# Kernel tuning notes

Measured on AMD Instinct MI355X. Metric: run time of the kernel, lower is better.

## Reference

```python
import jax, jax.numpy as jnp
import numpy as np

HEADS = 16
DIM_HEAD = 64
SCALE = 8.0
NUM_NULL_KV = 2
NON_CAUSAL_PREFIX = 64
LN_EPS = 1e-5

def _l2norm(t):
    # F.normalize: t / max(||t||_2, eps)
    n = jnp.sqrt(jnp.sum(t * t, axis=-1, keepdims=True))
    return t / jnp.maximum(n, 1e-12)

def _layer_norm(x, gamma):
    mu = jnp.mean(x, axis=-1, keepdims=True)
    var = jnp.mean((x - mu) ** 2, axis=-1, keepdims=True)
    return (x - mu) * jax.lax.rsqrt(var + LN_EPS) * gamma  # beta buffer is zeros

def setup_inputs() -> dict:
    key = jax.random.key(0)
    ks = jax.random.split(key, 6)
    b, n, dim = 2, 2048, 1024
    inner = HEADS * DIM_HEAD
    return {
        "x": jax.random.normal(ks[0], (b, n, dim), jnp.float32),
        "gamma": jnp.ones((dim,), jnp.float32),
        "Wq": jax.random.normal(ks[1], (dim, inner), jnp.float32) * (dim ** -0.5),
        "Wkv": jax.random.normal(ks[2], (dim, 2 * DIM_HEAD), jnp.float32) * (dim ** -0.5),
        "q_scale": jnp.ones((DIM_HEAD,), jnp.float32),
        "k_scale": jnp.ones((DIM_HEAD,), jnp.float32),
        "null_kv": jax.random.normal(ks[3], (2, NUM_NULL_KV, DIM_HEAD), jnp.float32),
        "Wout": jax.random.normal(ks[4], (inner, dim), jnp.float32) * (inner ** -0.5),
    }

def reference(x, gamma, Wq, Wkv, q_scale, k_scale, null_kv, Wout):
    b, n, dim = x.shape
    # NOTE: in the torch module, kv_input = x BEFORE self.norm is applied
    kv = jnp.einsum('bnd,de->bne', x, Wkv)          # [b, n, 2*dh]
    k, v = kv[..., :DIM_HEAD], kv[..., DIM_HEAD:]    # single shared kv head (MQA)
    xn = _layer_norm(x, gamma)
    q = jnp.einsum('bnd,de->bne', xn, Wq)            # [b, n, h*dh]
    # null kv prepended
    null_k = jnp.broadcast_to(null_kv[0], (b, NUM_NULL_KV, DIM_HEAD))
    null_v = jnp.broadcast_to(null_kv[1], (b, NUM_NULL_KV, DIM_HEAD))
    k = jnp.concatenate([null_k, k], axis=1)         # [b, j, dh]
    v = jnp.concatenate([null_v, v], axis=1)
    q = q.reshape(b, n, HEADS, DIM_HEAD).transpose(0, 2, 1, 3)  # [b, h, n, dh]
    q = _l2norm(q) * q_scale
    k = _l2norm(k) * k_scale
    sim = jnp.einsum('bhid,bjd->bhij', q, k) * SCALE  # [b, h, i, j]
    i, j = n, k.shape[1]
    rows = jnp.arange(i)[:, None]
    cols = jnp.arange(j)[None, :]
    causal_mask = cols > rows + (j - i)               # triu(j - i + 1)
    prefix_free = (rows < NON_CAUSAL_PREFIX) & (cols < NON_CAUSAL_PREFIX + (j - i))
    causal_mask = causal_mask & (~prefix_free)
    neg = -jnp.finfo(sim.dtype).max
    sim = jnp.where(causal_mask, neg, sim)
    attn = jax.nn.softmax(sim, axis=-1)
    out = jnp.einsum('bhij,bjd->bhid', attn, v)       # [b, h, n, dh]
    out = out.transpose(0, 2, 1, 3).reshape(b, n, HEADS * DIM_HEAD)
    return jnp.einsum('bne,ed->bnd', out, Wout)
```

## Files before the change

### kernel.cpp

```cpp
#include <hip/hip_runtime.h>

typedef _Float16 h16;
typedef _Float16 f16x8 __attribute__((ext_vector_type(8)));
typedef _Float16 f16x4 __attribute__((ext_vector_type(4)));
typedef float f32x4 __attribute__((ext_vector_type(4)));

#define KSCALE_FOLD 11.541560327111707f

#if __has_builtin(__builtin_amdgcn_exp2f)
#define EXP2(x) __builtin_amdgcn_exp2f(x)
#else
static __device__ __forceinline__ float EXP2(float x) {
    float r; asm("v_exp_f32 %0, %1" : "=v"(r) : "v"(x)); return r;
}
#endif

__global__ __launch_bounds__(256) void pre_k(const float* __restrict__ Wq,
    const float* __restrict__ Wkv, const float* __restrict__ Wout,
    const float* __restrict__ gamma, const float* __restrict__ x,
    const float* __restrict__ nkv, const float* __restrict__ kscale,
    h16* __restrict__ W1t, h16* __restrict__ Wot, float* __restrict__ cqp,
    float* __restrict__ mu, float* __restrict__ rr, h16* __restrict__ xh,
    h16* __restrict__ Kh, h16* __restrict__ Vth)
{
    __shared__ float ts[64][65];
    int pid = blockIdx.x;
    int tid = threadIdx.x;
    if (pid < 544) {
        int bx = pid & 15, by = pid >> 4;
        int c = tid & 63, rc = tid >> 6;
        const float* src; int ld, scol, drow0; h16* dst; bool useg = false;
        if (by < 16)      { src = Wq;   ld = 1024; scol = by*64;       dst = W1t; drow0 = scol;        useg = true; }
        else if (by < 18) { src = Wkv;  ld = 128;  scol = (by-16)*64;  dst = W1t; drow0 = 1024 + scol; }
        else              { src = Wout; ld = 1024; scol = (by-18)*64;  dst = Wot; drow0 = scol; }
        float part = 0.f;
#pragma unroll
        for (int i = 0; i < 16; ++i) {
            int r = rc*16 + i;
            float v = src[(size_t)(bx*64 + r)*ld + scol + c];
            if (useg) v *= gamma[bx*64 + r];
            part += v;
            ts[r][c] = v;
        }
        __syncthreads();
#pragma unroll
        for (int i = 0; i < 16; ++i) {
            int r = rc*16 + i;
            dst[(size_t)(drow0 + r)*1024 + bx*64 + c] = (h16)ts[c][r];
        }
        if (useg) {
            __syncthreads();
            ts[rc][c] = part;
            __syncthreads();
            if (rc == 0) {
                float s = ts[0][c] + ts[1][c] + ts[2][c] + ts[3][c];
                cqp[(size_t)bx*1024 + scol + c] = s;
            }
        }
    } else if (pid < 1568) {
        int w = tid >> 6, l = tid & 63;
        int row = (pid - 544)*4 + w;
        const float* xr = x + (size_t)row*1024;
        float s = 0.f, ss = 0.f;
        float4 v[4];
#pragma unroll
        for (int i = 0; i < 4; ++i) {
            v[i] = *(const float4*)(xr + i*256 + l*4);
            s  += v[i].x + v[i].y + v[i].z + v[i].w;
            ss += v[i].x*v[i].x + v[i].y*v[i].y + v[i].z*v[i].z + v[i].w*v[i].w;
        }
#pragma unroll
        for (int m = 1; m < 64; m <<= 1) { s += __shfl_xor(s, m); ss += __shfl_xor(ss, m); }
        float m_ = s * (1.f/1024.f);
        float var = ss * (1.f/1024.f) - m_*m_;
        float r_ = rsqrtf(var + 1e-5f);
        if (l == 0) { mu[row] = m_; rr[row] = r_; }
        h16* xo = xh + (size_t)row*1024;
#pragma unroll
        for (int i = 0; i < 4; ++i) {
            f16x4 hv = { (h16)v[i].x, (h16)v[i].y, (h16)v[i].z, (h16)v[i].w };
            *(f16x4*)(xo + i*256 + l*4) = hv;
        }
    } else {
        int nb = pid - 1568;
        if (nb == 0 && tid < 128) {
            int t = tid >> 6, d = tid & 63;
            float kv = nkv[(0*2 + t)*64 + d];
            float ss = kv*kv;
#pragma unroll
            for (int m = 1; m < 64; m <<= 1) ss += __shfl_xor(ss, m);
            float inv = 1.f / fmaxf(sqrtf(ss), 1e-12f);
            h16 kvh = (h16)(kv * inv * kscale[d] * KSCALE_FOLD);
            Kh[(size_t)(0*2112 + t)*64 + d] = kvh;
            Kh[(size_t)(1*2112 + t)*64 + d] = kvh;
            float nv = nkv[(2 + t)*64 + d];
            Vth[(size_t)(0*64 + d)*2112 + t] = (h16)nv;
            Vth[(size_t)(1*64 + d)*2112 + t] = (h16)nv;
        }
        for (int idx = nb*256 + tid; idx < 2*62*64; idx += 2048) {
            int b = idx / (62*64), rem = idx % (62*64);
            int j = 2050 + rem/64, d = rem & 63;
            Kh[((size_t)b*2112 + j)*64 + d] = (h16)0.f;
            Vth[((size_t)b*64 + d)*2112 + j] = (h16)0.f;
        }
    }
}

template<int MODE>
__global__ __launch_bounds__(256) void gemm_k(
    const h16* __restrict__ A, const h16* __restrict__ B,
    const float* __restrict__ mu, const float* __restrict__ rr, const float* __restrict__ cqp,
    const float* __restrict__ qscale, const float* __restrict__ kscale,
    h16* __restrict__ Qh, h16* __restrict__ Kh, h16* __restrict__ Vth, float* __restrict__ outp)
{
    __shared__ h16 As[2][128*64];
    __shared__ h16 Bs[2][64*64];
    int tid = threadIdx.x;
    int w = tid >> 6, l = tid & 63;
    int lq = l & 15, qq = l >> 4;
    int arow0 = blockIdx.y*128, bcol0 = blockIdx.x*64;
    const int K = 1024;
    f32x4 acc[2][4] = {};

    auto STAGE = [&](int buf, int kt) {
#pragma unroll
        for (int i = 0; i < 4; ++i) {
            int s = i*256 + tid;
            int row = s >> 3;
            int cb = ((s & 7)*16) ^ ((row & 7) << 4);
            const char* asrc = (const char*)(A + (size_t)(arow0 + row)*K + kt) + cb;
            __builtin_amdgcn_global_load_lds(
                (const __attribute__((address_space(1))) unsigned int*)asrc,
                (__attribute__((address_space(3))) unsigned int*)((char*)&As[buf][0] + s*16), 16, 0, 0);
        }
#pragma unroll
        for (int i = 0; i < 2; ++i) {
            int s = i*256 + tid;
            int row = s >> 3;
            int cb = ((s & 7)*16) ^ ((row & 7) << 4);
            const char* bsrc = (const char*)(B + (size_t)(bcol0 + row)*K + kt) + cb;
            __builtin_amdgcn_global_load_lds(
                (const __attribute__((address_space(1))) unsigned int*)bsrc,
                (__attribute__((address_space(3))) unsigned int*)((char*)&Bs[buf][0] + s*16), 16, 0, 0);
        }
    };

    STAGE(0, 0);
    int cur = 0;
    for (int kt = 0; kt < K; kt += 64) {
        int nkt = (kt + 64 < K) ? kt + 64 : kt;
        STAGE(cur ^ 1, nkt);
        asm volatile("s_waitcnt vmcnt(6)" ::: "memory");
        __builtin_amdgcn_s_barrier();
        __builtin_amdgcn_sched_barrier(0);
        const char* Ab = (const char*)&As[cur][0];
        const char* Bb = (const char*)&Bs[cur][0];
#pragma unroll
        for (int kc = 0; kc < 2; ++kc) {
            int cb = (kc*64 + qq*16) ^ ((lq & 7) << 4);
            f16x8 af[2], bf[4];
#pragma unroll
            for (int mt = 0; mt < 2; ++mt)
                af[mt] = *(const f16x8*)(Ab + (w*32 + mt*16 + lq)*128 + cb);
#pragma unroll
            for (int nt = 0; nt < 4; ++nt)
                bf[nt] = *(const f16x8*)(Bb + (nt*16 + lq)*128 + cb);
#pragma unroll
            for (int mt = 0; mt < 2; ++mt)
#pragma unroll
                for (int nt = 0; nt < 4; ++nt)
                    acc[mt][nt] = __builtin_amdgcn_mfma_f32_16x16x32_f16(af[mt], bf[nt], acc[mt][nt], 0, 0, 0);
        }
        __builtin_amdgcn_sched_barrier(0);
        __builtin_amdgcn_s_barrier();
        cur ^= 1;
    }
    asm volatile("s_waitcnt vmcnt(0)" ::: "memory");

    int wrow0 = arow0 + w*32;
    int bx = blockIdx.x;
    if (MODE == 1) {
#pragma unroll
        for (int mt = 0; mt < 2; ++mt)
#pragma unroll
            for (int nt = 0; nt < 4; ++nt)
#pragma unroll
                for (int i = 0; i < 4; ++i)
                    outp[(size_t)(wrow0 + mt*16 + qq*4 + i)*1024 + bcol0 + nt*16 + lq] = acc[mt][nt][i];
        return;
    }
    if (bx < 16) {
        float cqv[4], qs[4];
#pragma unroll
        for (int nt = 0; nt < 4; ++nt) {
            int col = bcol0 + nt*16 + lq;
            float s = 0.f;
#pragma unroll
            for (int j = 0; j < 16; ++j) s += cqp[(size_t)j*1024 + col];
            cqv[nt] = s;
            qs[nt] = qscale[nt*16 + lq];
        }
#pragma unroll
        for (int mt = 0; mt < 2; ++mt) {
            float muv[4], rv[4], ssq[4], qv[4][4];
#pragma unroll
            for (int i = 0; i < 4; ++i) {
                int row = wrow0 + mt*16 + qq*4 + i;
                muv[i] = mu[row]; rv[i] = rr[row]; ssq[i] = 0.f;
            }
#pragma unroll
            for (int nt = 0; nt < 4; ++nt)
#pragma unroll
                for (int i = 0; i < 4; ++i) {
                    float q = rv[i]*(acc[mt][nt][i] - muv[i]*cqv[nt]);
                    qv[nt][i] = q; ssq[i] += q*q;
                }
#pragma unroll
            for (int i = 0; i < 4; ++i) {
                float s2 = ssq[i];
                s2 += __shfl_xor(s2, 1); s2 += __shfl_xor(s2, 2);
                s2 += __shfl_xor(s2, 4); s2 += __shfl_xor(s2, 8);
                ssq[i] = 1.f / fmaxf(sqrtf(s2), 1e-12f);
            }
#pragma unroll
            for (int nt = 0; nt < 4; ++nt)
#pragma unroll
                for (int i = 0; i < 4; ++i) {
                    int row = wrow0 + mt*16 + qq*4 + i;
                    Qh[(size_t)row*1024 + bcol0 + nt*16 + lq] = (h16)(qv[nt][i]*ssq[i]*qs[nt]);
                }
        }
    } else if (bx == 16) {
        float ks[4];
#pragma unroll
        for (int nt = 0; nt < 4; ++nt) ks[nt] = kscale[nt*16 + lq] * KSCALE_FOLD;
#pragma unroll
        for (int mt = 0; mt < 2; ++mt) {
            float ssq[4] = {0.f, 0.f, 0.f, 0.f};
#pragma unroll
            for (int nt = 0; nt < 4; ++nt)
#pragma unroll
                for (int i = 0; i < 4; ++i) ssq[i] += acc[mt][nt][i]*acc[mt][nt][i];
#pragma unroll
            for (int i = 0; i < 4; ++i) {
                float s2 = ssq[i];
                s2 += __shfl_xor(s2, 1); s2 += __shfl_xor(s2, 2);
                s2 += __shfl_xor(s2, 4); s2 += __shfl_xor(s2, 8);
                ssq[i] = 1.f / fmaxf(sqrtf(s2), 1e-12f);
            }
#pragma unroll
            for (int nt = 0; nt < 4; ++nt)
#pragma unroll
                for (int i = 0; i < 4; ++i) {
                    int row = wrow0 + mt*16 + qq*4 + i;
                    int b = row >> 11, ii = row & 2047;
                    Kh[((size_t)b*2112 + 2 + ii)*64 + nt*16 + lq] = (h16)(acc[mt][nt][i]*ssq[i]*ks[nt]);
                }
        }
    } else {
#pragma unroll
        for (int mt = 0; mt < 2; ++mt)
#pragma unroll
            for (int nt = 0; nt < 4; ++nt)
#pragma unroll
                for (int i = 0; i < 4; ++i) {
                    int row = wrow0 + mt*16 + qq*4 + i;
                    int b = row >> 11, ii = row & 2047;
                    Vth[((size_t)b*64 + nt*16 + lq)*2112 + 2 + ii] = (h16)acc[mt][nt][i];
                }
    }
}

__global__ __launch_bounds__(256, 4) void attn_k(const h16* __restrict__ Qh,
    const h16* __restrict__ Kh, const h16* __restrict__ Vth, h16* __restrict__ Oh)
{
    __shared__ h16 KVs[2][2][64*64];
    __shared__ h16 Ps[4][16*64];
    int id = blockIdx.x;
    int u = id >> 5;
    int qt = (u < 16) ? u : 47 - u;
    int bh = id & 31;
    int b = bh >> 4, h = bh & 15;
    int tid = threadIdx.x, w = tid >> 6, l = tid & 63;
    int lq = l & 15, qq = l >> 4;
    int qstart = qt * 64;
    int q0w = qstart + w * 16;
    h16* P = &Ps[w][0];
    int xs = (lq & 7) << 4;

    f16x8 qf[2];
#pragma unroll
    for (int kc = 0; kc < 2; ++kc)
        qf[kc] = *(const f16x8*)(Qh + (size_t)(b*2048 + q0w + lq)*1024 + h*64 + kc*32 + qq*8);

    f16x8 ones;
#pragma unroll
    for (int i = 0; i < 8; ++i) ones[i] = (h16)1.f;

    int qrow = q0w + lq;
    int thr = (qrow < 64) ? 65 : qrow + 2;

    int cbs = ((tid & 7)*16) ^ (((tid >> 3) & 7) << 4);
    const char* ksrc = (const char*)(Kh + (size_t)b*2112*64) + (size_t)(tid >> 3)*128 + cbs;
    const char* vsrc = (const char*)(Vth + (size_t)b*64*2112) + (size_t)(tid >> 3)*4224 + cbs;

    f32x4 oacc[4] = {};
    f32x4 sacc = {};

    int lastc = qstart + 65;
    if (lastc > 2049) lastc = 2049;
    int ntile = lastc/64 + 1;

    auto STAGE = [&](int buf, int kv0) {
        const char* ks = ksrc + (size_t)kv0 * 128;
        const char* vs = vsrc + (size_t)kv0 * 2;
        __builtin_amdgcn_global_load_lds((const __attribute__((address_space(1))) unsigned int*)ks,
            (__attribute__((address_space(3))) unsigned int*)(&KVs[buf][0][(w*8)*64]), 16, 0, 0);
        __builtin_amdgcn_global_load_lds((const __attribute__((address_space(1))) unsigned int*)(ks + 32*128),
            (__attribute__((address_space(3))) unsigned int*)(&KVs[buf][0][(32 + w*8)*64]), 16, 0, 0);
        __builtin_amdgcn_global_load_lds((const __attribute__((address_space(1))) unsigned int*)vs,
            (__attribute__((address_space(3))) unsigned int*)(&KVs[buf][1][(w*8)*64]), 16, 0, 0);
        __builtin_amdgcn_global_load_lds((const __attribute__((address_space(1))) unsigned int*)(vs + (size_t)32*4224),
            (__attribute__((address_space(3))) unsigned int*)(&KVs[buf][1][(32 + w*8)*64]), 16, 0, 0);
    };

    STAGE(0, 0);
    int cur = 0;
    for (int t = 0; t < ntile; ++t) {
        int kv0 = t*64;
        int nxt = (t + 1 < ntile) ? t + 1 : t;
        STAGE(cur ^ 1, nxt*64);
        asm volatile("s_waitcnt vmcnt(4)" ::: "memory");
        __builtin_amdgcn_s_barrier();
        __builtin_amdgcn_sched_barrier(0);

        bool active = (kv0 <= q0w + 17) || (q0w < 64 && kv0 < 66);
        if (active) {
            const char* Kl = (const char*)&KVs[cur][0][0];
            const char* Vl = (const char*)&KVs[cur][1][0];
            f32x4 s[4] = {};
#pragma unroll
            for (int kc = 0; kc < 2; ++kc) {
                int ko = (kc*64 + qq*16) ^ xs;
                f16x8 kf[4];
#pragma unroll
                for (int mt = 0; mt < 4; ++mt)
                    kf[mt] = *(const f16x8*)(Kl + (mt*16 + lq)*128 + ko);
#pragma unroll
                for (int mt = 0; mt < 4; ++mt)
                    s[mt] = __builtin_amdgcn_mfma_f32_16x16x32_f16(kf[mt], qf[kc], s[mt], 0, 0, 0);
            }
            if (kv0 + 63 > q0w + 2) {
#pragma unroll
                for (int mt = 0; mt < 4; ++mt)
#pragma unroll
                    for (int i = 0; i < 4; ++i) {
                        int kv = kv0 + mt*16 + qq*4 + i;
                        if (kv > thr) s[mt][i] = -__builtin_inff();
                    }
            }
#pragma unroll
            for (int mt = 0; mt < 4; ++mt)
#pragma unroll
                for (int i = 0; i < 4; ++i)
                    s[mt][i] = EXP2(s[mt][i]);
#pragma unroll
            for (int mt = 0; mt < 4; ++mt) {
                uint2 pk;
                pk.x = __builtin_bit_cast(unsigned int, __builtin_amdgcn_cvt_pkrtz(s[mt][0], s[mt][1]));
                pk.y = __builtin_bit_cast(unsigned int, __builtin_amdgcn_cvt_pkrtz(s[mt][2], s[mt][3]));
                *(uint2*)((char*)P + lq*128 + ((mt*32 + qq*8) ^ xs)) = pk;
            }
#pragma unroll
            for (int kc = 0; kc < 2; ++kc) {
                int ko = (kc*64 + qq*16) ^ xs;
                f16x8 pf = *(const f16x8*)((const char*)P + lq*128 + ko);
#pragma unroll
                for (int dm = 0; dm < 4; ++dm) {
                    f16x8 vf = *(const f16x8*)(Vl + (dm*16 + lq)*128 + ko);
                    oacc[dm] = __builtin_amdgcn_mfma_f32_16x16x32_f16(vf, pf, oacc[dm], 0, 0, 0);
                }
                sacc = __builtin_amdgcn_mfma_f32_16x16x32_f16(ones, pf, sacc, 0, 0, 0);
            }
        }
        __builtin_amdgcn_sched_barrier(0);
        __builtin_amdgcn_s_barrier();
        cur ^= 1;
    }
    asm volatile("s_waitcnt vmcnt(0)" ::: "memory");

    float inv = 1.f / sacc[0];
#pragma unroll
    for (int dm = 0; dm < 4; ++dm) {
        f16x4 ov;
#pragma unroll
        for (int i = 0; i < 4; ++i) ov[i] = (h16)(oacc[dm][i]*inv);
        *(f16x4*)(Oh + (size_t)(b*2048 + q0w + lq)*1024 + h*64 + dm*16 + qq*4) = ov;
    }
}

extern "C" void kernel_launch(void* const* d_in, const int* in_sizes, int n_in,
                              void* d_out, int out_size, void* d_ws, size_t ws_size,
                              hipStream_t stream)
{
    const float* x      = (const float*)d_in[0];
    const float* gamma  = (const float*)d_in[1];
    const float* Wq     = (const float*)d_in[2];
    const float* Wkv    = (const float*)d_in[3];
    const float* qscale = (const float*)d_in[4];
    const float* kscale = (const float*)d_in[5];
    const float* nkv    = (const float*)d_in[6];
    const float* Wout   = (const float*)d_in[7];
    float* out = (float*)d_out;
    char* ws = (char*)d_ws;

    h16* xh    = (h16*)(ws);
    h16* Qh    = (h16*)(ws + 8388608);
    h16* Oh    = (h16*)(ws + 16777216);
    h16* W1t   = (h16*)(ws + 25165824);
    h16* Wot   = (h16*)(ws + 27525120);
    h16* Kh    = (h16*)(ws + 29622272);
    h16* Vth   = (h16*)(ws + 30162944);
    float* cqp = (float*)(ws + 30703616);
    float* mu  = (float*)(ws + 30769152);
    float* rr  = (float*)(ws + 30785536);

    pre_k<<<dim3(1576), 256, 0, stream>>>(Wq, Wkv, Wout, gamma, x, nkv, kscale,
                                          W1t, Wot, cqp, mu, rr, xh, Kh, Vth);
    gemm_k<0><<<dim3(18, 32), 256, 0, stream>>>(xh, W1t, mu, rr, cqp, qscale, kscale, Qh, Kh, Vth, out);
    attn_k<<<dim3(1024), 256, 0, stream>>>(Qh, Kh, Vth, Oh);
    gemm_k<1><<<dim3(16, 32), 256, 0, stream>>>(Oh, Wot, mu, rr, cqp, qscale, kscale, Qh, Kh, Vth, out);
}
```

Measured before the change: 86.08 us.

## Split KV range of long causal query tiles across two blocks and merge

Query tiles in the second half of the sequence now have their key/value range split into two halves, each handled by its own block, so the grid grows from 1024 to 1536 blocks. This shortens the critical path of the longest causal tiles. Each half writes a normalized partial output plus its softmax row sum (second half into reused xh workspace). A new merge kernel combines the two halves weighted by their sums, which works because the softmax here uses no running max. The cost is an extra launch, extra global traffic for the partials, and more blocks than fit in one wave.

```diff
diff --git a/kernel.cpp b/kernel.cpp
--- a/kernel.cpp
+++ b/kernel.cpp
@@ -272,15 +272,18 @@
 }
 
 __global__ __launch_bounds__(256, 4) void attn_k(const h16* __restrict__ Qh,
-    const h16* __restrict__ Kh, const h16* __restrict__ Vth, h16* __restrict__ Oh)
+    const h16* __restrict__ Kh, const h16* __restrict__ Vth, h16* __restrict__ Oh,
+    h16* __restrict__ OpB, float* __restrict__ LA, float* __restrict__ LB)
 {
     __shared__ h16 KVs[2][2][64*64];
     __shared__ h16 Ps[4][16*64];
     int id = blockIdx.x;
     int u = id >> 5;
-    int qt = (u < 16) ? u : 47 - u;
     int bh = id & 31;
     int b = bh >> 4, h = bh & 15;
+    int qt, half = 0; bool split = false;
+    if (u < 16) qt = u;
+    else { qt = 16 + ((u - 16) >> 1); half = (u - 16) & 1; split = true; }
     int tid = threadIdx.x, w = tid >> 6, l = tid & 63;
     int lq = l & 15, qq = l >> 4;
     int qstart = qt * 64;
@@ -310,6 +313,8 @@
     int lastc = qstart + 65;
     if (lastc > 2049) lastc = 2049;
     int ntile = lastc/64 + 1;
+    int t0 = 0, t1 = ntile;
+    if (split) { int hmid = ntile >> 1; if (half == 0) t1 = hmid; else t0 = hmid; }
 
     auto STAGE = [&](int buf, int kv0) {
         const char* ks = ksrc + (size_t)kv0 * 128;
@@ -324,11 +329,11 @@
             (__attribute__((address_space(3))) unsigned int*)(&KVs[buf][1][(32 + w*8)*64]), 16, 0, 0);
     };
 
-    STAGE(0, 0);
+    STAGE(0, t0*64);
     int cur = 0;
-    for (int t = 0; t < ntile; ++t) {
+    for (int t = t0; t < t1; ++t) {
         int kv0 = t*64;
-        int nxt = (t + 1 < ntile) ? t + 1 : t;
+        int nxt = (t + 1 < t1) ? t + 1 : t;
         STAGE(cur ^ 1, nxt*64);
         asm volatile("s_waitcnt vmcnt(4)" ::: "memory");
         __builtin_amdgcn_s_barrier();
@@ -389,14 +394,42 @@
     }
     asm volatile("s_waitcnt vmcnt(0)" ::: "memory");
 
-    float inv = 1.f / sacc[0];
+    float lsum = sacc[0];
+    float inv = 1.f / lsum;
+    h16* dst = (split && half == 1) ? OpB : Oh;
 #pragma unroll
     for (int dm = 0; dm < 4; ++dm) {
         f16x4 ov;
 #pragma unroll
         for (int i = 0; i < 4; ++i) ov[i] = (h16)(oacc[dm][i]*inv);
-        *(f16x4*)(Oh + (size_t)(b*2048 + q0w + lq)*1024 + h*64 + dm*16 + qq*4) = ov;
-    }
+        *(f16x4*)(dst + (size_t)(b*2048 + q0w + lq)*1024 + h*64 + dm*16 + qq*4) = ov;
+    }
+    if (split && qq == 0) {
+        int lrow = q0w + lq - 1024;
+        float* Lb = (half == 0) ? LA : LB;
+        Lb[(b*1024 + lrow)*16 + h] = lsum;
+    }
+}
+
+__global__ __launch_bounds__(256) void merge_k(h16* __restrict__ Oh,
+    const h16* __restrict__ OpB, const float* __restrict__ LA, const float* __restrict__ LB)
+{
+    int idx = blockIdx.x*256 + threadIdx.x;
+    int d0 = (idx & 7) * 8;
+    int h = (idx >> 3) & 15;
+    int lrow = (idx >> 7) & 1023;
+    int b = idx >> 17;
+    size_t off = ((size_t)(b*2048 + 1024 + lrow))*1024 + h*64 + d0;
+    float lA = LA[(b*1024 + lrow)*16 + h];
+    float lB = LB[(b*1024 + lrow)*16 + h];
+    float invt = 1.f / (lA + lB);
+    float wA = lA * invt, wB = lB * invt;
+    f16x8 a = *(const f16x8*)(Oh + off);
+    f16x8 c = *(const f16x8*)(OpB + off);
+    f16x8 o;
+#pragma unroll
+    for (int i = 0; i < 8; ++i) o[i] = (h16)((float)a[i]*wA + (float)c[i]*wB);
+    *(f16x8*)(Oh + off) = o;
 }
 
 extern "C" void kernel_launch(void* const* d_in, const int* in_sizes, int n_in,
@@ -425,9 +458,14 @@
     float* mu  = (float*)(ws + 30769152);
     float* rr  = (float*)(ws + 30785536);
 
+    float* LA = (float*)xh;
+    float* LB = (float*)((char*)xh + 131072);
+    h16*   OpB = xh;
+
     pre_k<<<dim3(1576), 256, 0, stream>>>(Wq, Wkv, Wout, gamma, x, nkv, kscale,
                                           W1t, Wot, cqp, mu, rr, xh, Kh, Vth);
     gemm_k<0><<<dim3(18, 32), 256, 0, stream>>>(xh, W1t, mu, rr, cqp, qscale, kscale, Qh, Kh, Vth, out);
-    attn_k<<<dim3(1024), 256, 0, stream>>>(Qh, Kh, Vth, Oh);
+    attn_k<<<dim3(1536), 256, 0, stream>>>(Qh, Kh, Vth, Oh, OpB, LA, LB);
+    merge_k<<<dim3(1024), 256, 0, stream>>>(Oh, OpB, LA, LB);
     gemm_k<1><<<dim3(16, 32), 256, 0, stream>>>(Oh, Wot, mu, rr, cqp, qscale, kscale, Qh, Kh, Vth, out);
 }
```

New measurement: 91.83 us. 6.7% more time.
